# Kernel tuning notes

Hardware: AMD Instinct MI355X
Metric: run time of the kernel (lower is better)

Reference implementation:

```python
import jax, jax.numpy as jnp
import numpy as np
from jax import lax

# dims: B batch, V views, D feature dim, C classes, P prompts
B, V, D, C, P = 512, 10, 1024, 100, 4
ADAPTER_RATIO = 0.6
EPS = 0.01          # sinkhorn entropic regularizer (compute_logits default)
MAX_ITER = 1000     # compute_logits default
THRESH = 1e-2       # PLOT Sinkhorn early-stop threshold on |r - r_prev|.mean()
BN_EPS = 1e-5


def setup_inputs() -> dict:
    key = jax.random.key(0)
    ks = jax.random.split(key, 8)
    # Correlated features so cosine similarity ~0.9 (realistic CLIP-like sims);
    # keeps exp(-wdist/0.01) well inside fp32 range for the Sinkhorn solver.
    base = jax.random.normal(ks[0], (D,), jnp.float32)
    feat = base[None, :] + 0.3 * jax.random.normal(ks[1], (B * V, D), jnp.float32)
    text_feat = base[None, None, :] + 0.3 * jax.random.normal(ks[2], (C, P, D), jnp.float32)
    w = lambda k, shp: 0.02 * jax.random.normal(k, shp, jnp.float32)
    return {
        "feat": feat,                       # (B*V, D) CLIP visual features
        "text_feat": text_feat,             # (C, P, D) encoded text features
        "fusion_ratio": jnp.full((V,), 0.5, jnp.float32),
        "bn1_gamma": jnp.ones((D,), jnp.float32),
        "bn1_beta": jnp.zeros((D,), jnp.float32),
        "W_glob": w(ks[3], (D, D * V)),     # Linear(D*V -> D), torch layout (out, in)
        "b_glob": jnp.zeros((D,), jnp.float32),
        "bn2_gamma": jnp.ones((D,), jnp.float32),
        "bn2_beta": jnp.zeros((D,), jnp.float32),
        "W_v1": w(ks[4], (D, D)),           # Linear(D -> D)
        "b_v1": jnp.zeros((D,), jnp.float32),
        "W_v2": w(ks[5], (D * V, D)),       # Linear(D -> D*V)
        "b_v2": jnp.zeros((D * V,), jnp.float32),
        "logit_scale": jnp.array(np.log(1.0 / 0.07), jnp.float32),
    }


def _bn_train(x, gamma, beta):
    # BatchNorm1d in training mode: biased batch statistics over axis 0
    m = x.mean(axis=0)
    v = x.var(axis=0)
    return (x - m) * lax.rsqrt(v + BN_EPS) * gamma + beta


def _adapter(feat, fusion_ratio, bn1_g, bn1_b, Wg, bg, bn2_g, bn2_b, Wv1, bv1, Wv2, bv2):
    img = feat.reshape(-1, V, D)
    res = feat.reshape(-1, V * D)
    x = img * fusion_ratio.reshape(1, -1, 1)          # per-view fusion weights
    x = _bn_train(x.reshape(-1, D), bn1_g, bn1_b)     # BatchNormPoint over D
    x = x.reshape(-1, V * D)                          # Flatten
    g = jax.nn.relu(_bn_train(x @ Wg.T + bg, bn2_g, bn2_b))   # global_f (dropout=0)
    view = jax.nn.relu(jax.nn.relu(g @ Wv1.T + bv1) @ Wv2.T + bv2)  # view_f
    return view * ADAPTER_RATIO + res * (1.0 - ADAPTER_RATIO)


def _sinkhorn(K, p, q):
    # PLOT-style Sinkhorn: r = p / (K c); c = q / (K^T r); early stop on mean |dr|
    r0 = jnp.ones_like(p)
    c0 = jnp.ones_like(q)

    def cond(st):
        i, r, c, err = st
        return jnp.logical_and(i < MAX_ITER, err > THRESH)

    def body(st):
        i, r, c, _ = st
        r_prev = r
        r = p / jnp.einsum('nvp,np->nv', K, c)
        c = q / jnp.einsum('nvp,nv->np', K, r)
        err = jnp.mean(jnp.abs(r - r_prev))
        return i + 1, r, c, err

    _, r, c, _ = lax.while_loop(cond, body, (jnp.int32(0), r0, c0, jnp.float32(jnp.inf)))
    return r[:, :, None] * K * c[:, None, :]   # T = diag(r) K diag(c)


def reference(feat, text_feat, fusion_ratio, bn1_gamma, bn1_beta, W_glob, b_glob,
              bn2_gamma, bn2_beta, W_v1, b_v1, W_v2, b_v2, logit_scale):
    img_feat = _adapter(feat, fusion_ratio, bn1_gamma, bn1_beta, W_glob, b_glob,
                        bn2_gamma, bn2_beta, W_v1, b_v1, W_v2, b_v2)
    img_feat = img_feat.reshape(-1, V, D)
    img_feat = img_feat / jnp.linalg.norm(img_feat, axis=-1, keepdims=True)
    txt = text_feat / jnp.linalg.norm(text_feat, axis=-1, keepdims=True)

    # compute_logits: sim (B, C, V, P) -> (B*C, V, P)
    sim = jnp.einsum('bvd,cpd->bcvp', img_feat, txt).reshape(B * C, V, P)
    wdist = 1.0 - sim
    p = jnp.full((B * C, V), 1.0 / V, sim.dtype)
    q = jnp.full((B * C, P), 1.0 / P, sim.dtype)
    K = jnp.exp(-wdist / EPS)
    T = _sinkhorn(lax.stop_gradient(K), p, q)   # solver runs under no_grad
    d_OT = jnp.sum(T * wdist, axis=(1, 2)).reshape(B, C)
    logits = jnp.exp(logit_scale) * (1.0 - d_OT)
    return logits
```

## Files before the change

### kernel.cpp

```cpp
#include <hip/hip_runtime.h>
#include <cstdint>


typedef unsigned short u16;
typedef __attribute__((ext_vector_type(8))) short bf8v;
typedef __attribute__((ext_vector_type(4))) float f4v;

__device__ __forceinline__ float4 ld4(const float* p){ return *reinterpret_cast<const float4*>(p); }
__device__ __forceinline__ void st4(float* p, float4 v){ *reinterpret_cast<float4*>(p) = v; }
__device__ __forceinline__ u16 f2bf(float x){
  uint32_t u = __float_as_uint(x);
  return (u16)((u + 0x7FFFu + ((u>>16)&1u)) >> 16);
}
__device__ __forceinline__ uint32_t pk(float a, float b){
  return (uint32_t)f2bf(a) | ((uint32_t)f2bf(b)<<16);
}
__device__ __forceinline__ void glds16(const u16* g, u16* l){
  __builtin_amdgcn_global_load_lds(
      (const __attribute__((address_space(1))) unsigned int*)g,
      (__attribute__((address_space(3))) unsigned int*)l, 16, 0, 0);
}

__global__ __launch_bounds__(256,4)
void gemm_bf16_nt(const u16* __restrict__ A, const u16* __restrict__ B,
                  float* __restrict__ C, int lda, int ldb, int ldc,
                  int kLen, long strideCz)
{
  __shared__ u16 As0[2048], Bs0[4096], As1[2048], Bs1[4096];
  const int tid = threadIdx.x, lane = tid & 63, w = tid >> 6;
  const long bm = (long)blockIdx.y*64, bn = (long)blockIdx.x*128;
  const long kz = (long)blockIdx.z*kLen;
  C += (long)blockIdx.z*strideCz;

  const int srow  = lane>>2;
  const int sslot = (lane&3) ^ ((lane>>3)&3);
  const u16* Ag = A + (bm + w*16 + srow)*(long)lda + kz + sslot*8;
  const u16* Bg = B + (bn + w*32 + srow)*(long)ldb + kz + sslot*8;
  const long b16 = 16L*ldb;
  const int woffA = w*512, woffB = w*1024;

  const int fr = lane & 15;
  const int rslot = ((lane>>4) ^ ((lane>>1)&3))*16;
  const int wr = (w>>1)*32, wc = (w&1)*64;

  const f4v zero = {0.f,0.f,0.f,0.f};
  f4v acc[2][4];
  #pragma unroll
  for (int i=0;i<2;i++)
    #pragma unroll
    for (int j=0;j<4;j++) acc[i][j]=zero;

  auto STAGE = [&](u16* Al, u16* Bl, int kt){
    glds16(Ag + kt,       Al + woffA);
    glds16(Bg + kt,       Bl + woffB);
    glds16(Bg + kt + b16, Bl + woffB + 512);
  };
  auto COMPUTE = [&](const u16* Asb, const u16* Bsb){
    bf8v af[2], bf[4];
    #pragma unroll
    for (int mi=0; mi<2; ++mi)
      af[mi] = *(const bf8v*)((const char*)Asb + (wr+mi*16+fr)*64 + rslot);
    #pragma unroll
    for (int nj=0; nj<4; ++nj)
      bf[nj] = *(const bf8v*)((const char*)Bsb + (wc+nj*16+fr)*64 + rslot);
    #pragma unroll
    for (int mi=0; mi<2; ++mi)
      #pragma unroll
      for (int nj=0; nj<4; ++nj)
        acc[mi][nj] = __builtin_amdgcn_mfma_f32_16x16x32_bf16(af[mi], bf[nj], acc[mi][nj], 0,0,0);
  };

  STAGE(As0, Bs0, 0);
  __syncthreads();
  int kt = 32;
  for (; kt < kLen - 32; kt += 64){
    STAGE(As1, Bs1, kt);
    COMPUTE(As0, Bs0);
    __syncthreads();
    STAGE(As0, Bs0, kt + 32);
    COMPUTE(As1, Bs1);
    __syncthreads();
  }
  STAGE(As1, Bs1, kt);
  COMPUTE(As0, Bs0);
  __syncthreads();
  COMPUTE(As1, Bs1);

  const int orow = (lane>>4)*4;
  #pragma unroll
  for (int mi=0;mi<2;++mi){
    #pragma unroll
    for (int q=0;q<4;++q){
      const long row = bm + wr + mi*16 + orow + q;
      float* Crow = C + row*(long)ldc + bn + wc + fr;
      #pragma unroll
      for (int nj=0;nj<4;++nj) Crow[nj*16] = acc[mi][nj][q];
    }
  }
}

__global__ __launch_bounds__(256,4)
void gemm_bf32b_nt(const u16* __restrict__ A, const float* __restrict__ B,
                   float* __restrict__ C, int lda, int ldb, int ldc,
                   int kLen, long strideCz)
{
  __shared__ u16 As0[2048], Bs0[4096], As1[2048], Bs1[4096];
  const int tid = threadIdx.x, lane = tid & 63, w = tid >> 6;
  const long bm = (long)blockIdx.y*64, bn = (long)blockIdx.x*128;
  const long kz = (long)blockIdx.z*kLen;
  C += (long)blockIdx.z*strideCz;

  const int srow  = lane>>2;
  const int sslot = (lane&3) ^ ((lane>>3)&3);
  const u16* Ag = A + (bm + w*16 + srow)*(long)lda + kz + sslot*8;
  const int woffA = w*512;

  const int rB = tid>>1, sp = (tid&1)<<1, mB = (rB>>1)&3;
  const float* Bg = B + (bn + rB)*(long)ldb + kz + sp*8;
  const int bo0 = rB*32 + ((sp  )^mB)*8;
  const int bo1 = rB*32 + ((sp+1)^mB)*8;

  const int fr = lane & 15;
  const int rslot = ((lane>>4) ^ ((lane>>1)&3))*16;
  const int wr = (w>>1)*32, wc = (w&1)*64;

  const f4v zero = {0.f,0.f,0.f,0.f};
  f4v acc[2][4];
  #pragma unroll
  for (int i=0;i<2;i++)
    #pragma unroll
    for (int j=0;j<4;j++) acc[i][j]=zero;

  float4 br0[4], br1[4];
  auto LOADB = [&](float4* r4, int kt){
    r4[0]=ld4(Bg+kt); r4[1]=ld4(Bg+kt+4); r4[2]=ld4(Bg+kt+8); r4[3]=ld4(Bg+kt+12);
  };
  auto WRITEB = [&](u16* Bsb, const float4* r4){
    uint4 o0, o1;
    o0.x=pk(r4[0].x,r4[0].y); o0.y=pk(r4[0].z,r4[0].w);
    o0.z=pk(r4[1].x,r4[1].y); o0.w=pk(r4[1].z,r4[1].w);
    o1.x=pk(r4[2].x,r4[2].y); o1.y=pk(r4[2].z,r4[2].w);
    o1.z=pk(r4[3].x,r4[3].y); o1.w=pk(r4[3].z,r4[3].w);
    *reinterpret_cast<uint4*>(&Bsb[bo0]) = o0;
    *reinterpret_cast<uint4*>(&Bsb[bo1]) = o1;
  };
  auto GLA = [&](u16* Al, int kt){ glds16(Ag + kt, Al + woffA); };
  auto COMPUTE = [&](const u16* Asb, const u16* Bsb){
    bf8v af[2], bf[4];
    #pragma unroll
    for (int mi=0; mi<2; ++mi)
      af[mi] = *(const bf8v*)((const char*)Asb + (wr+mi*16+fr)*64 + rslot);
    #pragma unroll
    for (int nj=0; nj<4; ++nj)
      bf[nj] = *(const bf8v*)((const char*)Bsb + (wc+nj*16+fr)*64 + rslot);
    #pragma unroll
    for (int mi=0; mi<2; ++mi)
      #pragma unroll
      for (int nj=0; nj<4; ++nj)
        acc[mi][nj] = __builtin_amdgcn_mfma_f32_16x16x32_bf16(af[mi], bf[nj], acc[mi][nj], 0,0,0);
  };

  LOADB(br0, 0); GLA(As0, 0);
  WRITEB(Bs0, br0);
  __syncthreads();
  int kt = 32;
  for (; kt < kLen - 32; kt += 64){
    LOADB(br1, kt); GLA(As1, kt);
    COMPUTE(As0, Bs0);
    WRITEB(Bs1, br1);
    __syncthreads();
    LOADB(br0, kt+32); GLA(As0, kt+32);
    COMPUTE(As1, Bs1);
    WRITEB(Bs0, br0);
    __syncthreads();
  }
  LOADB(br1, kt); GLA(As1, kt);
  COMPUTE(As0, Bs0);
  WRITEB(Bs1, br1);
  __syncthreads();
  COMPUTE(As1, Bs1);

  const int orow = (lane>>4)*4;
  #pragma unroll
  for (int mi=0;mi<2;++mi){
    #pragma unroll
    for (int q=0;q<4;++q){
      const long row = bm + wr + mi*16 + orow + q;
      float* Crow = C + row*(long)ldc + bn + wc + fr;
      #pragma unroll
      for (int nj=0;nj<4;++nj) Crow[nj*16] = acc[mi][nj][q];
    }
  }
}

__global__ __launch_bounds__(256)
void reduce_f32(const float* __restrict__ P, int S, int MN,
                const float* __restrict__ bias, float* __restrict__ out)
{
  const long i = ((long)blockIdx.x*256 + threadIdx.x)*4;
  float4 s = ld4(&P[i]);
  for (int z=1; z<S; ++z){
    const float4 v = ld4(&P[(long)z*MN + i]);
    s.x+=v.x; s.y+=v.y; s.z+=v.z; s.w+=v.w;
  }
  const float4 b = ld4(&bias[(int)(i & 1023)]);
  s.x+=b.x; s.y+=b.y; s.z+=b.z; s.w+=b.w;
  st4(&out[i], s);
}

__global__ __launch_bounds__(256)
void reduce_bf16(const float* __restrict__ P, int S, int MN,
                 const float* __restrict__ bias, u16* __restrict__ out)
{
  const long i = ((long)blockIdx.x*256 + threadIdx.x)*4;
  float4 s = ld4(&P[i]);
  for (int z=1; z<S; ++z){
    const float4 v = ld4(&P[(long)z*MN + i]);
    s.x+=v.x; s.y+=v.y; s.z+=v.z; s.w+=v.w;
  }
  const float4 b = ld4(&bias[(int)(i & 1023)]);
  s.x = fmaxf(s.x+b.x,0.f); s.y = fmaxf(s.y+b.y,0.f);
  s.z = fmaxf(s.z+b.z,0.f); s.w = fmaxf(s.w+b.w,0.f);
  uint2 o; o.x = pk(s.x,s.y); o.y = pk(s.z,s.w);
  *reinterpret_cast<uint2*>(&out[i]) = o;
}

__global__ __launch_bounds__(256)
void colstats_p1(const float* __restrict__ X, int rpb, const float* __restrict__ fr,
                 float* __restrict__ part)
{
  const int c = threadIdx.x*4;
  const long r0 = (long)blockIdx.x*rpb;
  float4 s = make_float4(0,0,0,0), q = make_float4(0,0,0,0);
  for (int rr=0; rr<rpb; ++rr){
    const long r = r0+rr;
    float4 x = ld4(&X[r*1024 + c]);
    if (fr){ const float f = fr[(int)(r%10)]; x.x*=f; x.y*=f; x.z*=f; x.w*=f; }
    s.x+=x.x; s.y+=x.y; s.z+=x.z; s.w+=x.w;
    q.x+=x.x*x.x; q.y+=x.y*x.y; q.z+=x.z*x.z; q.w+=x.w*x.w;
  }
  float* p = part + (long)blockIdx.x*2048;
  st4(&p[c], s);
  st4(&p[1024+c], q);
}

__global__ __launch_bounds__(256)
void colstats_reduce(const float* __restrict__ in, float* __restrict__ out,
                     int nslab, int chunk)
{
  const int idx = blockIdx.x*256 + threadIdx.x;
  const int s0 = blockIdx.y*chunk;
  const int s1 = min(nslab, s0+chunk);
  float a0=0.f, a1=0.f, a2=0.f, a3=0.f;
  int s = s0;
  for (; s+4 <= s1; s += 4){
    a0 += in[(long)s*2048+idx];
    a1 += in[(long)(s+1)*2048+idx];
    a2 += in[(long)(s+2)*2048+idx];
    a3 += in[(long)(s+3)*2048+idx];
  }
  for (; s < s1; ++s) a0 += in[(long)s*2048+idx];
  out[(long)blockIdx.y*2048 + idx] = (a0+a1)+(a2+a3);
}

__global__ __launch_bounds__(256)
void bn_apply_bf16(const float* __restrict__ X, const float* __restrict__ fr,
                   const float* __restrict__ stats, float invN,
                   const float* __restrict__ gamma,
                   const float* __restrict__ beta, int relu, u16* __restrict__ out)
{
  const long i = ((long)blockIdx.x*256 + threadIdx.x)*4;
  const int d = (int)(i & 1023);
  const float4 s  = ld4(&stats[d]);
  const float4 qq = ld4(&stats[1024+d]);
  const float4 gm = ld4(&gamma[d]);
  const float4 bt = ld4(&beta[d]);
  float4 sc, sh;
  { const float m=s.x*invN, v=qq.x*invN-m*m; sc.x=gm.x*rsqrtf(v+1e-5f); sh.x=bt.x-m*sc.x; }
  { const float m=s.y*invN, v=qq.y*invN-m*m; sc.y=gm.y*rsqrtf(v+1e-5f); sh.y=bt.y-m*sc.y; }
  { const float m=s.z*invN, v=qq.z*invN-m*m; sc.z=gm.z*rsqrtf(v+1e-5f); sh.z=bt.z-m*sc.z; }
  { const float m=s.w*invN, v=qq.w*invN-m*m; sc.w=gm.w*rsqrtf(v+1e-5f); sh.w=bt.w-m*sc.w; }
  float4 x = ld4(&X[i]);
  if (fr){ const float f = fr[(int)((i>>10)%10)]; x.x*=f; x.y*=f; x.z*=f; x.w*=f; }
  x.x = x.x*sc.x + sh.x; x.y = x.y*sc.y + sh.y;
  x.z = x.z*sc.z + sh.z; x.w = x.w*sc.w + sh.w;
  if (relu){ x.x=fmaxf(x.x,0.f); x.y=fmaxf(x.y,0.f); x.z=fmaxf(x.z,0.f); x.w=fmaxf(x.w,0.f); }
  uint2 o; o.x = pk(x.x,x.y); o.y = pk(x.z,x.w);
  *reinterpret_cast<uint2*>(&out[i]) = o;
}

__device__ __forceinline__ float blockSum256(float v, float* sh4){
  #pragma unroll
  for (int m=32; m; m>>=1) v += __shfl_xor(v, m, 64);
  const int w = threadIdx.x >> 6;
  if ((threadIdx.x & 63) == 0) sh4[w] = v;
  __syncthreads();
  return sh4[0]+sh4[1]+sh4[2]+sh4[3];
}

__global__ __launch_bounds__(256)
void rownorm_bf16(const float* __restrict__ X, u16* __restrict__ out)
{
  __shared__ float sh4[4];
  const int row = blockIdx.x;
  const int d = threadIdx.x*4;
  if (row >= 400){ *reinterpret_cast<uint2*>(&out[(long)row*1024 + d]) = make_uint2(0,0); return; }
  const long base = (long)row*1024 + d;
  const float4 x = ld4(&X[base]);
  const float ss = x.x*x.x + x.y*x.y + x.z*x.z + x.w*x.w;
  const float rn = rsqrtf(blockSum256(ss, sh4));
  uint2 o; o.x = pk(x.x*rn, x.y*rn); o.y = pk(x.z*rn, x.w*rn);
  *reinterpret_cast<uint2*>(&out[base]) = o;
}

__global__ __launch_bounds__(256)
void mix_norm_bf16(const float* __restrict__ P, const float* __restrict__ feat,
                   const float* __restrict__ bv2, u16* __restrict__ outp)
{
  __shared__ float sh4[4];
  const int m = blockIdx.x;
  const int v = m % 10;
  const long base = (long)m*1024;
  const int d = threadIdx.x*4;
  const float4 y  = ld4(&P[base+d]);
  const float4 bb = ld4(&bv2[v*1024 + d]);
  const float4 f  = ld4(&feat[base+d]);
  float4 img;
  img.x = 0.6f*fmaxf(y.x+bb.x,0.f) + 0.4f*f.x;
  img.y = 0.6f*fmaxf(y.y+bb.y,0.f) + 0.4f*f.y;
  img.z = 0.6f*fmaxf(y.z+bb.z,0.f) + 0.4f*f.z;
  img.w = 0.6f*fmaxf(y.w+bb.w,0.f) + 0.4f*f.w;
  const float ss = img.x*img.x + img.y*img.y + img.z*img.z + img.w*img.w;
  const float rn = rsqrtf(blockSum256(ss, sh4));
  uint2 o; o.x = pk(img.x*rn, img.y*rn); o.y = pk(img.z*rn, img.w*rn);
  *reinterpret_cast<uint2*>(&outp[base+d]) = o;
}

__global__ __launch_bounds__(256)
void sinkhorn_solve(const float* __restrict__ sim, const float* __restrict__ lsp,
                    float* __restrict__ out)
{
  const int n = blockIdx.x*256 + threadIdx.x;
  const int b = n / 100, c = n % 100;
  float S[10][4], Km[10][4];
  #pragma unroll
  for (int v=0; v<10; ++v){
    const long off = (long)(b*10+v)*512 + c*4;
    const float4 a0 = ld4(&sim[off]);
    const float4 a1 = ld4(&sim[2621440L + off]);
    S[v][0]=a0.x+a1.x; S[v][1]=a0.y+a1.y; S[v][2]=a0.z+a1.z; S[v][3]=a0.w+a1.w;
    #pragma unroll
    for (int p=0;p<4;++p) Km[v][p] = expf((S[v][p]-1.f)*100.f);
  }
  float r[10], cc[4];
  #pragma unroll
  for (int v=0;v<10;++v) r[v]=1.f;
  #pragma unroll
  for (int p=0;p<4;++p) cc[p]=1.f;
  for (int j=0; j<1000; ++j){
    float lerr = 0.f;
    #pragma unroll
    for (int v=0;v<10;++v){
      const float s = Km[v][0]*cc[0]+Km[v][1]*cc[1]+Km[v][2]*cc[2]+Km[v][3]*cc[3];
      const float rn = __fdividef(0.1f, s);
      lerr += fabsf(rn - r[v]); r[v]=rn;
    }
    #pragma unroll
    for (int p=0;p<4;++p){
      float s = 0.f;
      #pragma unroll
      for (int v=0;v<10;++v) s += Km[v][p]*r[v];
      cc[p] = __fdividef(0.25f, s);
    }
    float w = lerr;
    #pragma unroll
    for (int m=32; m; m>>=1) w += __shfl_xor(w, m, 64);
    if (w <= 0.25f) break;
  }
  float dOT = 0.f;
  #pragma unroll
  for (int v=0;v<10;++v)
    #pragma unroll
    for (int p=0;p<4;++p)
      dOT += r[v]*Km[v][p]*cc[p]*(1.f - S[v][p]);
  out[n] = expf(lsp[0]) * (1.f - dOT);
}

extern "C" void kernel_launch(void* const* d_in, const int* in_sizes, int n_in,
                              void* d_out, int out_size, void* d_ws, size_t ws_size,
                              hipStream_t stream)
{
  const float* feat  = (const float*)d_in[0];
  const float* textf = (const float*)d_in[1];
  const float* fr    = (const float*)d_in[2];
  const float* bn1g  = (const float*)d_in[3];
  const float* bn1b  = (const float*)d_in[4];
  const float* Wg    = (const float*)d_in[5];
  const float* bg    = (const float*)d_in[6];
  const float* bn2g  = (const float*)d_in[7];
  const float* bn2b  = (const float*)d_in[8];
  const float* Wv1   = (const float*)d_in[9];
  const float* bv1   = (const float*)d_in[10];
  const float* Wv2   = (const float*)d_in[11];
  const float* bv2   = (const float*)d_in[12];
  const float* ls    = (const float*)d_in[13];
  float* out = (float*)d_out;
  char* base = (char*)d_ws;

  u16*   Xb  = (u16*)(base + 20971520);
  float* P   = (float*)(base + 31457280);
  float* P2  = P + 1310720;
  float* y1  = (float*)(base + 67108864);
  u16*   Gb  = (u16*)(base + 69206016);
  u16*   Hb  = (u16*)(base + 70254592);
  u16*   Tb  = (u16*)(base + 71303168);
  float* ex  = (float*)(base + 72351744);
  float* bn1st=ex, *bn2st=ex+2048;

  colstats_p1<<<640,256,0,stream>>>(feat, 8, fr, P);
  colstats_reduce<<<dim3(8,20),256,0,stream>>>(P, P2, 640, 32);
  colstats_reduce<<<dim3(8,1),256,0,stream>>>(P2, bn1st, 20, 20);
  bn_apply_bf16<<<5120,256,0,stream>>>(feat, fr, bn1st, 1.f/5120.f,
                                       bn1g, bn1b, 0, Xb);

  gemm_bf32b_nt<<<dim3(8,8,16),256,0,stream>>>(Xb, Wg, P, 10240,10240,1024, 640, 524288L);
  reduce_f32<<<512,256,0,stream>>>(P, 16, 524288, bg, y1);

  colstats_p1<<<128,256,0,stream>>>(y1, 4, nullptr, P);
  colstats_reduce<<<dim3(8,8),256,0,stream>>>(P, P2, 128, 16);
  colstats_reduce<<<dim3(8,1),256,0,stream>>>(P2, bn2st, 8, 8);
  bn_apply_bf16<<<512,256,0,stream>>>(y1, nullptr, bn2st, 1.f/512.f,
                                      bn2g, bn2b, 1, Gb);

  gemm_bf32b_nt<<<dim3(8,8,16),256,0,stream>>>(Gb, Wv1, P, 1024,1024,1024, 64, 524288L);
  reduce_bf16<<<512,256,0,stream>>>(P, 16, 524288, bv1, Hb);

  gemm_bf32b_nt<<<dim3(80,8,1),256,0,stream>>>(Hb, Wv2, P, 1024,1024,10240, 1024, 0L);
  mix_norm_bf16<<<5120,256,0,stream>>>(P, feat, bv2, Xb);

  rownorm_bf16<<<512,256,0,stream>>>(textf, Tb);
  gemm_bf16_nt<<<dim3(4,80,2),256,0,stream>>>(Xb, Tb, P, 1024,1024,512, 512, 2621440L);

  sinkhorn_solve<<<200,256,0,stream>>>(P, ls, out);
}
```

Before: 172.6 us.

## Pre-convert fp32 weights to bf16 and remap GEMM blocks per XCD

Three fp32-weight GEMMs now run after a separate cvt_bf16 pass that writes bf16 copies of W_glob, W_v1 and W_v2. This lets all GEMMs use the bf16 global_load_lds kernel, and the fused fp32-load-and-pack variant is removed. GEMM launches become 1D grids whose block index is remapped so blocks sharing a split-K slice or N range land on the same XCD, aiming for better L2 reuse. The W_v1 GEMM split-K drops from 16 to 8. The cost is extra conversion kernels that read fp32 weights and write bf16 copies every call.

```diff
diff --git a/kernel.cpp b/kernel.cpp
--- a/kernel.cpp
+++ b/kernel.cpp
@@ -24,13 +24,29 @@
 __global__ __launch_bounds__(256,4)
 void gemm_bf16_nt(const u16* __restrict__ A, const u16* __restrict__ B,
                   float* __restrict__ C, int lda, int ldb, int ldc,
-                  int kLen, long strideCz)
+                  int kLen, long strideCz, int map, int NBX, int NBY)
 {
   __shared__ u16 As0[2048], Bs0[4096], As1[2048], Bs1[4096];
   const int tid = threadIdx.x, lane = tid & 63, w = tid >> 6;
-  const long bm = (long)blockIdx.y*64, bn = (long)blockIdx.x*128;
-  const long kz = (long)blockIdx.z*kLen;
-  C += (long)blockIdx.z*strideCz;
+
+  int bx, by, bz;
+  if (map == 0){ bx = blockIdx.x; by = blockIdx.y; bz = blockIdx.z; }
+  else {
+    const int i = blockIdx.x, xcd = i & 7, j = i >> 3;
+    if (map == 1){
+      const int mnC = NBX*NBY;
+      const int zPer = (gridDim.x >> 3) / mnC;
+      bz = xcd*zPer + j/mnC;
+      const int mn = j % mnC; bx = mn % NBX; by = mn / NBX;
+    } else {
+      const int nbxPer = NBX >> 3;
+      bx = xcd*nbxPer + j % nbxPer; by = j / nbxPer; bz = 0;
+    }
+  }
+
+  const long bm = (long)by*64, bn = (long)bx*128;
+  const long kz = (long)bz*kLen;
+  C += (long)bz*strideCz;
 
   const int srow  = lane>>2;
   const int sslot = (lane&3) ^ ((lane>>3)&3);
@@ -46,9 +62,9 @@
   const f4v zero = {0.f,0.f,0.f,0.f};
   f4v acc[2][4];
   #pragma unroll
-  for (int i=0;i<2;i++)
-    #pragma unroll
-    for (int j=0;j<4;j++) acc[i][j]=zero;
+  for (int i2=0;i2<2;i2++)
+    #pragma unroll
+    for (int j2=0;j2<4;j2++) acc[i2][j2]=zero;
 
   auto STAGE = [&](u16* Al, u16* Bl, int kt){
     glds16(Ag + kt,       Al + woffA);
@@ -99,97 +115,15 @@
   }
 }
 
-__global__ __launch_bounds__(256,4)
-void gemm_bf32b_nt(const u16* __restrict__ A, const float* __restrict__ B,
-                   float* __restrict__ C, int lda, int ldb, int ldc,
-                   int kLen, long strideCz)
-{
-  __shared__ u16 As0[2048], Bs0[4096], As1[2048], Bs1[4096];
-  const int tid = threadIdx.x, lane = tid & 63, w = tid >> 6;
-  const long bm = (long)blockIdx.y*64, bn = (long)blockIdx.x*128;
-  const long kz = (long)blockIdx.z*kLen;
-  C += (long)blockIdx.z*strideCz;
-
-  const int srow  = lane>>2;
-  const int sslot = (lane&3) ^ ((lane>>3)&3);
-  const u16* Ag = A + (bm + w*16 + srow)*(long)lda + kz + sslot*8;
-  const int woffA = w*512;
-
-  const int rB = tid>>1, sp = (tid&1)<<1, mB = (rB>>1)&3;
-  const float* Bg = B + (bn + rB)*(long)ldb + kz + sp*8;
-  const int bo0 = rB*32 + ((sp  )^mB)*8;
-  const int bo1 = rB*32 + ((sp+1)^mB)*8;
-
-  const int fr = lane & 15;
-  const int rslot = ((lane>>4) ^ ((lane>>1)&3))*16;
-  const int wr = (w>>1)*32, wc = (w&1)*64;
-
-  const f4v zero = {0.f,0.f,0.f,0.f};
-  f4v acc[2][4];
-  #pragma unroll
-  for (int i=0;i<2;i++)
-    #pragma unroll
-    for (int j=0;j<4;j++) acc[i][j]=zero;
-
-  float4 br0[4], br1[4];
-  auto LOADB = [&](float4* r4, int kt){
-    r4[0]=ld4(Bg+kt); r4[1]=ld4(Bg+kt+4); r4[2]=ld4(Bg+kt+8); r4[3]=ld4(Bg+kt+12);
-  };
-  auto WRITEB = [&](u16* Bsb, const float4* r4){
-    uint4 o0, o1;
-    o0.x=pk(r4[0].x,r4[0].y); o0.y=pk(r4[0].z,r4[0].w);
-    o0.z=pk(r4[1].x,r4[1].y); o0.w=pk(r4[1].z,r4[1].w);
-    o1.x=pk(r4[2].x,r4[2].y); o1.y=pk(r4[2].z,r4[2].w);
-    o1.z=pk(r4[3].x,r4[3].y); o1.w=pk(r4[3].z,r4[3].w);
-    *reinterpret_cast<uint4*>(&Bsb[bo0]) = o0;
-    *reinterpret_cast<uint4*>(&Bsb[bo1]) = o1;
-  };
-  auto GLA = [&](u16* Al, int kt){ glds16(Ag + kt, Al + woffA); };
-  auto COMPUTE = [&](const u16* Asb, const u16* Bsb){
-    bf8v af[2], bf[4];
-    #pragma unroll
-    for (int mi=0; mi<2; ++mi)
-      af[mi] = *(const bf8v*)((const char*)Asb + (wr+mi*16+fr)*64 + rslot);
-    #pragma unroll
-    for (int nj=0; nj<4; ++nj)
-      bf[nj] = *(const bf8v*)((const char*)Bsb + (wc+nj*16+fr)*64 + rslot);
-    #pragma unroll
-    for (int mi=0; mi<2; ++mi)
-      #pragma unroll
-      for (int nj=0; nj<4; ++nj)
-        acc[mi][nj] = __builtin_amdgcn_mfma_f32_16x16x32_bf16(af[mi], bf[nj], acc[mi][nj], 0,0,0);
-  };
-
-  LOADB(br0, 0); GLA(As0, 0);
-  WRITEB(Bs0, br0);
-  __syncthreads();
-  int kt = 32;
-  for (; kt < kLen - 32; kt += 64){
-    LOADB(br1, kt); GLA(As1, kt);
-    COMPUTE(As0, Bs0);
-    WRITEB(Bs1, br1);
-    __syncthreads();
-    LOADB(br0, kt+32); GLA(As0, kt+32);
-    COMPUTE(As1, Bs1);
-    WRITEB(Bs0, br0);
-    __syncthreads();
-  }
-  LOADB(br1, kt); GLA(As1, kt);
-  COMPUTE(As0, Bs0);
-  WRITEB(Bs1, br1);
-  __syncthreads();
-  COMPUTE(As1, Bs1);
-
-  const int orow = (lane>>4)*4;
-  #pragma unroll
-  for (int mi=0;mi<2;++mi){
-    #pragma unroll
-    for (int q=0;q<4;++q){
-      const long row = bm + wr + mi*16 + orow + q;
-      float* Crow = C + row*(long)ldc + bn + wc + fr;
-      #pragma unroll
-      for (int nj=0;nj<4;++nj) Crow[nj*16] = acc[mi][nj][q];
-    }
+__global__ __launch_bounds__(256)
+void cvt_bf16(const float* __restrict__ in, u16* __restrict__ out, long n8)
+{
+  for (long i = (long)blockIdx.x*256 + threadIdx.x; i < n8; i += (long)gridDim.x*256){
+    const float4 a = ld4(&in[i*8]), b = ld4(&in[i*8+4]);
+    uint4 o;
+    o.x = pk(a.x,a.y); o.y = pk(a.z,a.w);
+    o.z = pk(b.x,b.y); o.w = pk(b.z,b.w);
+    *reinterpret_cast<uint4*>(&out[i*8]) = o;
   }
 }
 
@@ -407,9 +341,11 @@
   float* out = (float*)d_out;
   char* base = (char*)d_ws;
 
+  u16*   WB  = (u16*)(base + 0);
   u16*   Xb  = (u16*)(base + 20971520);
   float* P   = (float*)(base + 31457280);
   float* P2  = P + 1310720;
+  u16*   W1b = (u16*)(base + 65011712);
   float* y1  = (float*)(base + 67108864);
   u16*   Gb  = (u16*)(base + 69206016);
   u16*   Hb  = (u16*)(base + 70254592);
@@ -417,13 +353,16 @@
   float* ex  = (float*)(base + 72351744);
   float* bn1st=ex, *bn2st=ex+2048;
 
+  cvt_bf16<<<2048,256,0,stream>>>(Wg, WB, 1310720);
+
   colstats_p1<<<640,256,0,stream>>>(feat, 8, fr, P);
   colstats_reduce<<<dim3(8,20),256,0,stream>>>(P, P2, 640, 32);
   colstats_reduce<<<dim3(8,1),256,0,stream>>>(P2, bn1st, 20, 20);
   bn_apply_bf16<<<5120,256,0,stream>>>(feat, fr, bn1st, 1.f/5120.f,
                                        bn1g, bn1b, 0, Xb);
 
-  gemm_bf32b_nt<<<dim3(8,8,16),256,0,stream>>>(Xb, Wg, P, 10240,10240,1024, 640, 524288L);
+  gemm_bf16_nt<<<1024,256,0,stream>>>(Xb, WB, P, 10240,10240,1024, 640, 524288L,
+                                      1, 8, 8);
   reduce_f32<<<512,256,0,stream>>>(P, 16, 524288, bg, y1);
 
   colstats_p1<<<128,256,0,stream>>>(y1, 4, nullptr, P);
@@ -431,15 +370,21 @@
   colstats_reduce<<<dim3(8,1),256,0,stream>>>(P2, bn2st, 8, 8);
   bn_apply_bf16<<<512,256,0,stream>>>(y1, nullptr, bn2st, 1.f/512.f,
                                       bn2g, bn2b, 1, Gb);
-
-  gemm_bf32b_nt<<<dim3(8,8,16),256,0,stream>>>(Gb, Wv1, P, 1024,1024,1024, 64, 524288L);
-  reduce_bf16<<<512,256,0,stream>>>(P, 16, 524288, bv1, Hb);
-
-  gemm_bf32b_nt<<<dim3(80,8,1),256,0,stream>>>(Hb, Wv2, P, 1024,1024,10240, 1024, 0L);
+  cvt_bf16<<<512,256,0,stream>>>(Wv1, W1b, 131072);
+
+  gemm_bf16_nt<<<512,256,0,stream>>>(Gb, W1b, P, 1024,1024,1024, 128, 524288L,
+                                     1, 8, 8);
+  reduce_bf16<<<512,256,0,stream>>>(P, 8, 524288, bv1, Hb);
+
+  cvt_bf16<<<2048,256,0,stream>>>(Wv2, WB, 1310720);
+
+  gemm_bf16_nt<<<640,256,0,stream>>>(Hb, WB, P, 1024,1024,10240, 1024, 0L,
+                                     2, 80, 8);
   mix_norm_bf16<<<5120,256,0,stream>>>(P, feat, bv2, Xb);
 
   rownorm_bf16<<<512,256,0,stream>>>(textf, Tb);
-  gemm_bf16_nt<<<dim3(4,80,2),256,0,stream>>>(Xb, Tb, P, 1024,1024,512, 512, 2621440L);
+  gemm_bf16_nt<<<dim3(4,80,2),256,0,stream>>>(Xb, Tb, P, 1024,1024,512, 512,
+                                              2621440L, 0, 0, 0);
 
   sinkhorn_solve<<<200,256,0,stream>>>(P, ls, out);
 }
```

New measurement: 152.8 us. 11.5% less time.
